# Performance work log

Hardware: AMD Instinct MI355X
Metric: run time of the kernel (lower is better)

Reference implementation:

```python
import jax, jax.numpy as jnp
import numpy as np

N_NODES = 100000
N_EDGES = 1000000
IN_DIM = 64
HID = 64
OUT_DIM = 32
NUM_GRAPHS = 512


def setup_inputs() -> dict:
    key = jax.random.key(0)
    ks = jax.random.split(key, 16)
    x = jax.random.normal(ks[0], (N_NODES, IN_DIM), dtype=jnp.float32)
    edge_index = jax.random.randint(ks[1], (2, N_EDGES), 0, N_NODES, dtype=jnp.int64)
    batch = jnp.sort(jax.random.randint(ks[2], (N_NODES,), 0, NUM_GRAPHS, dtype=jnp.int64))

    def lin(k, i, o):
        s = 1.0 / np.sqrt(i)
        kw, kb = jax.random.split(k)
        return (jax.random.uniform(kw, (i, o), jnp.float32, -s, s),
                jax.random.uniform(kb, (o,), jnp.float32, -s, s))

    W1a, b1a = lin(ks[3], IN_DIM, HID)
    W2a, b2a = lin(ks[4], HID, HID)
    W1b, b1b = lin(ks[5], HID, HID)
    W2b, b2b = lin(ks[6], HID, HID)
    Wp1, bp1 = lin(ks[7], HID, HID)
    Wp2, bp2 = lin(ks[8], HID, OUT_DIM)
    return dict(x=x, edge_index=edge_index, batch=batch,
                W1a=W1a, b1a=b1a, W2a=W2a, b2a=b2a,
                W1b=W1b, b1b=b1b, W2b=W2b, b2b=b2b,
                Wp1=Wp1, bp1=bp1, Wp2=Wp2, bp2=bp2)


def _gin_layer(x, edge_index, W1, b1, W2, b2):
    # GINConv (eps=0): h_i = MLP(x_i + sum_{j->i} x_j)
    src, dst = edge_index[0], edge_index[1]
    agg = jax.ops.segment_sum(x[src], dst, num_segments=N_NODES)  # [N, d]
    h = x + agg
    h = jnp.maximum(h @ W1 + b1, 0.0) @ W2 + b2
    return h


def reference(x, edge_index, batch,
              W1a, b1a, W2a, b2a,
              W1b, b1b, W2b, b2b,
              Wp1, bp1, Wp2, bp2):
    # layer 0 (dropout is identity in eval mode)
    x = _gin_layer(x, edge_index, W1a, b1a, W2a, b2a)
    x = jnp.maximum(x, 0.0)
    # layer 1
    x = _gin_layer(x, edge_index, W1b, b1b, W2b, b2b)
    emb = x  # pre-ReLU embedding of last executed conv
    x = jnp.maximum(x, 0.0)
    # global mean pool over graphs
    sums = jax.ops.segment_sum(x, batch, num_segments=NUM_GRAPHS)  # [G, d]
    cnts = jax.ops.segment_sum(jnp.ones((x.shape[0],), x.dtype), batch, num_segments=NUM_GRAPHS)
    pooled = sums / jnp.maximum(cnts, 1.0)[:, None]
    # post-MLP (dropout identity in eval)
    out = (pooled @ Wp1 + bp1) @ Wp2 + bp2
    return emb, jax.nn.log_softmax(out, axis=1)
```

## Files before the change

kernel.cpp:

```cpp
#include <hip/hip_runtime.h>
#include <math.h>

#define N_NODES 100000
#define N_EDGES 1000000
#define HID 64
#define OUT_DIM 32
#define NUM_GRAPHS 512
#define CAP 48
#define NBUCK 98
#define BCAP 11264
#define ACHUNK 4096

typedef __attribute__((ext_vector_type(4))) float f4v;
typedef __attribute__((ext_vector_type(4))) int i4v;
typedef __attribute__((ext_vector_type(8))) short s8v;
typedef __attribute__((ext_vector_type(4))) short s4vs;

static __device__ inline short f2bf(float f) {
  unsigned u = __float_as_uint(f);
  unsigned r = (u + 0x7fffu + ((u >> 16) & 1u)) >> 16;
  return (short)r;
}
static __device__ inline float bf2f(short s) {
  return __uint_as_float(((unsigned)(unsigned short)s) << 16);
}

__global__ __launch_bounds__(256) void prep_kernel(
    const float* __restrict__ W1a, const float* __restrict__ W2a,
    const float* __restrict__ W1b, const float* __restrict__ W2b,
    short* __restrict__ wtab, const int* __restrict__ batch,
    int* __restrict__ starts, int* __restrict__ bcnt) {
  int t = blockIdx.x * 256 + threadIdx.x;
  if (t < 16384) {
    int which = t >> 12;
    int r = t & 4095;
    const float* W = (which == 0) ? W1a : (which == 1) ? W2a : (which == 2) ? W1b : W2b;
    short* hiT = wtab + which * 8192;
    short* loT = hiT + 4096;
    int n = r & 63, k = r >> 6;
    float w = W[k * HID + n];
    short h = f2bf(w);
    hiT[n * HID + k] = h;
    loT[n * HID + k] = f2bf(w - bf2f(h));
  } else if (t < 16384 + NUM_GRAPHS + 1) {
    int g = t - 16384;
    int lo = 0, hi = N_NODES;
    while (lo < hi) {
      int mid = (lo + hi) >> 1;
      if (batch[mid] < g) lo = mid + 1; else hi = mid;
    }
    starts[g] = lo;
  } else if (t < 16384 + NUM_GRAPHS + 1 + NBUCK) {
    bcnt[t - 16384 - NUM_GRAPHS - 1] = 0;
  }
}

__global__ __launch_bounds__(256) void bucket_kernel(
    const int* __restrict__ ei, int* __restrict__ bedge,
    int* __restrict__ bcnt, int n_edges) {
  __shared__ int s_pack[ACHUNK];
  __shared__ unsigned char s_b[ACHUNK];
  __shared__ int s_sorted[ACHUNK];
  __shared__ int s_hist[NBUCK];
  __shared__ int s_off[NBUCK];
  __shared__ int s_base[NBUCK];

  int e0 = blockIdx.x * ACHUNK;
  int n = n_edges - e0;
  if (n > ACHUNK) n = ACHUNK;
  int tid = threadIdx.x;

  for (int i = tid; i < NBUCK; i += 256) s_hist[i] = 0;
  __syncthreads();

  for (int i = tid; i < n; i += 256) {
    int src = ei[e0 + i];
    int dst = ei[n_edges + e0 + i];
    int b = dst >> 10;
    s_pack[i] = src | ((dst & 1023) << 17);
    s_b[i] = (unsigned char)b;
    atomicAdd(&s_hist[b], 1);
  }
  __syncthreads();

  if (tid < NBUCK) s_off[tid] = s_hist[tid];
  __syncthreads();
  for (int off = 1; off < NBUCK; off <<= 1) {
    int v = 0;
    if (tid < NBUCK && tid >= off) v = s_off[tid - off];
    __syncthreads();
    if (tid < NBUCK && tid >= off) s_off[tid] += v;
    __syncthreads();
  }
  if (tid < NBUCK) {
    int excl = s_off[tid] - s_hist[tid];
    s_off[tid] = excl;
    int c = s_hist[tid];
    s_base[tid] = c > 0 ? atomicAdd(&bcnt[tid], c) : 0;
  }
  __syncthreads();

  for (int i = tid; i < n; i += 256) {
    int p = atomicAdd(&s_off[s_b[i]], 1);
    s_sorted[p] = s_pack[i];
  }
  __syncthreads();

  int wv = tid >> 6;
  int lane = tid & 63;
  for (int b = wv; b < NBUCK; b += 4) {
    int cnt = s_hist[b];
    if (cnt == 0) continue;
    int start = s_off[b] - cnt;
    int gbase = s_base[b];
    for (int i = lane; i < cnt; i += 64) {
      int idx = gbase + i;
      if (idx < BCAP) bedge[b * BCAP + idx] = s_sorted[start + i];
    }
  }
}

__global__ __launch_bounds__(256) void csr_from_buckets_kernel(
    const int* __restrict__ bedge, const int* __restrict__ bcnt,
    int* __restrict__ deg, int* __restrict__ csr) {
  __shared__ int ldeg[1024];
  int b = blockIdx.x;
  int tid = threadIdx.x;
  for (int i = tid; i < 1024; i += 256) ldeg[i] = 0;
  __syncthreads();

  int n = bcnt[b];
  if (n > BCAP) n = BCAP;
  const int* bb = bedge + b * BCAP;
  for (int i0 = tid * 4; i0 < n; i0 += 1024) {
    int e0, e1, e2, e3;
    int rem = n - i0;
    if (rem >= 4) {
      i4v v = *(const i4v*)(bb + i0);
      e0 = v.x; e1 = v.y; e2 = v.z; e3 = v.w;
    } else {
      e0 = bb[i0];
      e1 = (rem > 1) ? bb[i0 + 1] : 0;
      e2 = (rem > 2) ? bb[i0 + 2] : 0;
      e3 = 0;
    }
    {
      int local = e0 >> 17, src = e0 & 0x1FFFF;
      int slot = atomicAdd(&ldeg[local], 1);
      if (slot < CAP) csr[(((size_t)b << 10) | local) * CAP + slot] = src;
    }
    if (n - i0 > 1) {
      int local = e1 >> 17, src = e1 & 0x1FFFF;
      int slot = atomicAdd(&ldeg[local], 1);
      if (slot < CAP) csr[(((size_t)b << 10) | local) * CAP + slot] = src;
    }
    if (n - i0 > 2) {
      int local = e2 >> 17, src = e2 & 0x1FFFF;
      int slot = atomicAdd(&ldeg[local], 1);
      if (slot < CAP) csr[(((size_t)b << 10) | local) * CAP + slot] = src;
    }
    if (n - i0 > 3) {
      int local = e3 >> 17, src = e3 & 0x1FFFF;
      int slot = atomicAdd(&ldeg[local], 1);
      if (slot < CAP) csr[(((size_t)b << 10) | local) * CAP + slot] = src;
    }
  }
  __syncthreads();

  for (int i = tid; i < 1024; i += 256) {
    int node = (b << 10) + i;
    if (node < N_NODES) deg[node] = ldeg[i];
  }
}

__global__ __launch_bounds__(256) void gather_kernel(
    const float* __restrict__ x, const int* __restrict__ deg,
    const int* __restrict__ csr, short* __restrict__ hbufHi,
    short* __restrict__ hbufLo, int n_nodes) {
  int lane = threadIdx.x & 63;
  int node = blockIdx.x * (blockDim.x >> 6) + (threadIdx.x >> 6);
  if (node >= n_nodes) return;
  int g = lane >> 4;
  int sub = lane & 15;

  const f4v* x4 = (const f4v*)x;
  f4v a0 = (g == 0) ? x4[(size_t)node * 16 + sub] : (f4v){0.f, 0.f, 0.f, 0.f};
  int idx = (lane < 16) ? csr[node * CAP + lane] : 0;
  int d = deg[node];
  if (d > CAP) d = CAP;

  f4v a1 = {0.f, 0.f, 0.f, 0.f};
  f4v a2 = {0.f, 0.f, 0.f, 0.f};
  f4v a3 = {0.f, 0.f, 0.f, 0.f};
  if (d > 0) {
    int j1 = g, j2 = 4 + g, j3 = 8 + g, j4 = 12 + g;
    int s1 = __shfl(idx, j1);
    int s2 = __shfl(idx, j2);
    int s3 = __shfl(idx, j3);
    int s4 = __shfl(idx, j4);
    if (j1 < d) a0 += x4[(size_t)s1 * 16 + sub];
    if (j2 < d) a1 += x4[(size_t)s2 * 16 + sub];
    if (j3 < d) a2 += x4[(size_t)s3 * 16 + sub];
    if (j4 < d) a3 += x4[(size_t)s4 * 16 + sub];
  }
  if (d > 16) {
    int idx2 = (lane < 32) ? csr[node * CAP + 16 + lane] : 0;
    for (int j0 = 16; j0 < d; j0 += 16) {
      int j1 = j0 + g, j2 = j0 + 4 + g, j3 = j0 + 8 + g, j4 = j0 + 12 + g;
      int s1 = __shfl(idx2, j1 - 16);
      int s2 = __shfl(idx2, j2 - 16);
      int s3 = __shfl(idx2, j3 - 16);
      int s4 = __shfl(idx2, j4 - 16);
      if (j1 < d) a0 += x4[(size_t)s1 * 16 + sub];
      if (j2 < d) a1 += x4[(size_t)s2 * 16 + sub];
      if (j3 < d) a2 += x4[(size_t)s3 * 16 + sub];
      if (j4 < d) a3 += x4[(size_t)s4 * 16 + sub];
    }
  }
  f4v a = (a0 + a1) + (a2 + a3);
  a.x += __shfl_xor(a.x, 16); a.y += __shfl_xor(a.y, 16);
  a.z += __shfl_xor(a.z, 16); a.w += __shfl_xor(a.w, 16);
  a.x += __shfl_xor(a.x, 32); a.y += __shfl_xor(a.y, 32);
  a.z += __shfl_xor(a.z, 32); a.w += __shfl_xor(a.w, 32);
  if (g == 0) {
    s4vs hi, lo;
#pragma unroll
    for (int c = 0; c < 4; c++) {
      float v = a[c];
      short hb = f2bf(v);
      hi[c] = hb;
      lo[c] = f2bf(v - bf2f(hb));
    }
    ((s4vs*)hbufHi)[(size_t)node * 16 + sub] = hi;
    ((s4vs*)hbufLo)[(size_t)node * 16 + sub] = lo;
  }
}

#define LPAD 72

__global__ __launch_bounds__(256) void gin_mlp_mfma_kernel(
    const short* __restrict__ hbufHi, const short* __restrict__ hbufLo,
    const short* __restrict__ W1hi, const short* __restrict__ W1lo,
    const float* __restrict__ b1,
    const short* __restrict__ W2hi, const short* __restrict__ W2lo,
    const float* __restrict__ b2,
    float* __restrict__ out, int n_nodes, int apply_relu) {
  __shared__ short lds[4][2][16 * LPAD];

  int lane = threadIdx.x & 63;
  int wv = threadIdx.x >> 6;
  int m = lane & 15;
  int quad = lane >> 4;
  int nodeBase = blockIdx.x * 64 + wv * 16;
  int node = nodeBase + m;
  bool valid = node < n_nodes;

  s8v ahi[2], alo[2];
#pragma unroll
  for (int kb = 0; kb < 2; kb++) {
    int off = node * HID + kb * 32 + quad * 8;
    if (valid) {
      ahi[kb] = *(const s8v*)(hbufHi + off);
      alo[kb] = *(const s8v*)(hbufLo + off);
    } else {
      ahi[kb] = (s8v){0, 0, 0, 0, 0, 0, 0, 0};
      alo[kb] = (s8v){0, 0, 0, 0, 0, 0, 0, 0};
    }
  }

  f4v acc[4];
#pragma unroll
  for (int nt = 0; nt < 4; nt++) acc[nt] = (f4v){0.f, 0.f, 0.f, 0.f};
#pragma unroll
  for (int kb = 0; kb < 2; kb++) {
#pragma unroll
    for (int nt = 0; nt < 4; nt++) {
      int n = nt * 16 + m;
      s8v bh = *(const s8v*)(W1hi + n * HID + kb * 32 + quad * 8);
      s8v bl = *(const s8v*)(W1lo + n * HID + kb * 32 + quad * 8);
      acc[nt] = __builtin_amdgcn_mfma_f32_16x16x32_bf16(ahi[kb], bh, acc[nt], 0, 0, 0);
      acc[nt] = __builtin_amdgcn_mfma_f32_16x16x32_bf16(ahi[kb], bl, acc[nt], 0, 0, 0);
      acc[nt] = __builtin_amdgcn_mfma_f32_16x16x32_bf16(alo[kb], bh, acc[nt], 0, 0, 0);
      acc[nt] = __builtin_amdgcn_mfma_f32_16x16x32_bf16(alo[kb], bl, acc[nt], 0, 0, 0);
    }
  }

  short* Lhi = lds[wv][0];
  short* Llo = lds[wv][1];
#pragma unroll
  for (int nt = 0; nt < 4; nt++) {
    int col = nt * 16 + m;
    float bb = b1[col];
#pragma unroll
    for (int r = 0; r < 4; r++) {
      int row = quad * 4 + r;
      float h = fmaxf(acc[nt][r] + bb, 0.f);
      short hb = f2bf(h);
      Lhi[row * LPAD + col] = hb;
      Llo[row * LPAD + col] = f2bf(h - bf2f(hb));
    }
  }
  __syncthreads();

  s8v a2hi[2], a2lo[2];
#pragma unroll
  for (int kb = 0; kb < 2; kb++) {
    int off = m * LPAD + kb * 32 + quad * 8;
    a2hi[kb] = *(const s8v*)(Lhi + off);
    a2lo[kb] = *(const s8v*)(Llo + off);
  }

  f4v acc2[4];
#pragma unroll
  for (int nt = 0; nt < 4; nt++) acc2[nt] = (f4v){0.f, 0.f, 0.f, 0.f};
#pragma unroll
  for (int kb = 0; kb < 2; kb++) {
#pragma unroll
    for (int nt = 0; nt < 4; nt++) {
      int n = nt * 16 + m;
      s8v bh = *(const s8v*)(W2hi + n * HID + kb * 32 + quad * 8);
      s8v bl = *(const s8v*)(W2lo + n * HID + kb * 32 + quad * 8);
      acc2[nt] = __builtin_amdgcn_mfma_f32_16x16x32_bf16(a2hi[kb], bh, acc2[nt], 0, 0, 0);
      acc2[nt] = __builtin_amdgcn_mfma_f32_16x16x32_bf16(a2hi[kb], bl, acc2[nt], 0, 0, 0);
      acc2[nt] = __builtin_amdgcn_mfma_f32_16x16x32_bf16(a2lo[kb], bh, acc2[nt], 0, 0, 0);
      acc2[nt] = __builtin_amdgcn_mfma_f32_16x16x32_bf16(a2lo[kb], bl, acc2[nt], 0, 0, 0);
    }
  }

#pragma unroll
  for (int nt = 0; nt < 4; nt++) {
    int col = nt * 16 + m;
    float bb = b2[col];
#pragma unroll
    for (int r = 0; r < 4; r++) {
      int row = quad * 4 + r;
      int onode = nodeBase + row;
      if (onode < n_nodes) {
        float o = acc2[nt][r] + bb;
        if (apply_relu) o = fmaxf(o, 0.f);
        out[(size_t)onode * HID + col] = o;
      }
    }
  }
}

__global__ __launch_bounds__(256) void poolhead_kernel(
    const float* __restrict__ emb, const int* __restrict__ starts,
    const float* __restrict__ Wp1, const float* __restrict__ bp1,
    const float* __restrict__ Wp2, const float* __restrict__ bp2,
    float* __restrict__ out) {
  int lane = threadIdx.x & 63;
  int g = blockIdx.x * 4 + (threadIdx.x >> 6);
  int group = lane >> 4, sub = lane & 15;
  int s0 = starts[g], s1 = starts[g + 1];

  const f4v* e4 = (const f4v*)emb;
  f4v acc = {0.f, 0.f, 0.f, 0.f};
  for (int n = s0 + group; n < s1; n += 4) {
    f4v v = e4[(size_t)n * 16 + sub];
    v.x = fmaxf(v.x, 0.f); v.y = fmaxf(v.y, 0.f);
    v.z = fmaxf(v.z, 0.f); v.w = fmaxf(v.w, 0.f);
    acc += v;
  }
  acc.x += __shfl_xor(acc.x, 16); acc.y += __shfl_xor(acc.y, 16);
  acc.z += __shfl_xor(acc.z, 16); acc.w += __shfl_xor(acc.w, 16);
  acc.x += __shfl_xor(acc.x, 32); acc.y += __shfl_xor(acc.y, 32);
  acc.z += __shfl_xor(acc.z, 32); acc.w += __shfl_xor(acc.w, 32);
  int srcl = lane >> 2;
  float v0 = __shfl(acc.x, srcl);
  float v1 = __shfl(acc.y, srcl);
  float v2 = __shfl(acc.z, srcl);
  float v3 = __shfl(acc.w, srcl);
  int r = lane & 3;
  float psum = (r == 0) ? v0 : (r == 1) ? v1 : (r == 2) ? v2 : v3;

  float c = fmaxf((float)(s1 - s0), 1.0f);
  float p = psum / c;

  float t = bp1[lane];
#pragma unroll
  for (int k = 0; k < HID; k++) {
    t += __shfl(p, k) * Wp1[k * HID + lane];
  }

  float acc2 = 0.0f;
#pragma unroll
  for (int k = 0; k < HID; k++) {
    float tk = __shfl(t, k);
    if (lane < OUT_DIM) acc2 += tk * Wp2[k * OUT_DIM + lane];
  }
  float o = (lane < OUT_DIM) ? (acc2 + bp2[lane]) : -1e30f;

  float m = o;
#pragma unroll
  for (int off = 32; off >= 1; off >>= 1) m = fmaxf(m, __shfl_xor(m, off));
  float ex = (lane < OUT_DIM) ? expf(o - m) : 0.0f;
  float s = ex;
#pragma unroll
  for (int off = 32; off >= 1; off >>= 1) s += __shfl_xor(s, off);
  float lse = m + logf(s);
  if (lane < OUT_DIM) out[g * OUT_DIM + lane] = o - lse;
}

extern "C" void kernel_launch(void* const* d_in, const int* in_sizes, int n_in,
                              void* d_out, int out_size, void* d_ws, size_t ws_size,
                              hipStream_t stream) {
  const float* x   = (const float*)d_in[0];
  const int* ei    = (const int*)d_in[1];
  const int* batch = (const int*)d_in[2];
  const float* W1a = (const float*)d_in[3];
  const float* b1a = (const float*)d_in[4];
  const float* W2a = (const float*)d_in[5];
  const float* b2a = (const float*)d_in[6];
  const float* W1b = (const float*)d_in[7];
  const float* b1b = (const float*)d_in[8];
  const float* W2b = (const float*)d_in[9];
  const float* b2b = (const float*)d_in[10];
  const float* Wp1 = (const float*)d_in[11];
  const float* bp1 = (const float*)d_in[12];
  const float* Wp2 = (const float*)d_in[13];
  const float* bp2 = (const float*)d_in[14];

  float* emb    = (float*)d_out;
  float* logits = (float*)d_out + (size_t)N_NODES * HID;
  float* x1 = emb;

  short* hbufHi = (short*)d_ws;
  short* hbufLo = hbufHi + (size_t)N_NODES * HID;
  int* bedge   = (int*)d_ws;
  int* bcnt    = bedge + NBUCK * BCAP;
  int* deg     = (int*)((float*)d_ws + (size_t)N_NODES * HID);
  int* csr     = deg + N_NODES;
  int* starts  = csr + (size_t)N_NODES * CAP;
  short* wtab  = (short*)(starts + NUM_GRAPHS + 1);
  short* W1aHi = wtab + 0 * 4096; short* W1aLo = wtab + 1 * 4096;
  short* W2aHi = wtab + 2 * 4096; short* W2aLo = wtab + 3 * 4096;
  short* W1bHi = wtab + 4 * 4096; short* W1bLo = wtab + 5 * 4096;
  short* W2bHi = wtab + 6 * 4096; short* W2bLo = wtab + 7 * 4096;

  int prep_threads = 16384 + (NUM_GRAPHS + 1) + NBUCK;
  prep_kernel<<<(prep_threads + 255) / 256, 256, 0, stream>>>(
      W1a, W2a, W1b, W2b, wtab, batch, starts, bcnt);

  bucket_kernel<<<(N_EDGES + ACHUNK - 1) / ACHUNK, 256, 0, stream>>>(
      ei, bedge, bcnt, N_EDGES);
  csr_from_buckets_kernel<<<NBUCK, 256, 0, stream>>>(bedge, bcnt, deg, csr);

  int gather_blocks = (N_NODES + 3) / 4;
  int mlp_blocks = (N_NODES + 63) / 64;

  gather_kernel<<<gather_blocks, 256, 0, stream>>>(
      x, deg, csr, hbufHi, hbufLo, N_NODES);
  gin_mlp_mfma_kernel<<<mlp_blocks, 256, 0, stream>>>(
      hbufHi, hbufLo, W1aHi, W1aLo, b1a, W2aHi, W2aLo, b2a, x1, N_NODES, 1);

  gather_kernel<<<gather_blocks, 256, 0, stream>>>(
      x1, deg, csr, hbufHi, hbufLo, N_NODES);
  gin_mlp_mfma_kernel<<<mlp_blocks, 256, 0, stream>>>(
      hbufHi, hbufLo, W1bHi, W1bLo, b1b, W2bHi, W2bLo, b2b, emb, N_NODES, 0);

  poolhead_kernel<<<NUM_GRAPHS / 4, 256, 0, stream>>>(
      emb, starts, Wp1, bp1, Wp2, bp2, logits);
}
```

Baseline: 322.7 us.

## Fuse prep into bucket kernel, drop lo*lo MFMA term, one graph per pool block

Merges the weight-split/graph-start prep kernel into the edge bucketing kernel as extra blocks, and replaces the bucket-count zeroing with a memset, saving one launch. Drops the lo×lo cross term from the split-bf16 MFMA products in both MLP layers, cutting a quarter of the matrix instructions at a tiny precision cost. Pool/head kernel now uses one 64-thread block per graph instead of four graphs per 256-thread block.

```diff
diff --git a/kernel.cpp b/kernel.cpp
--- a/kernel.cpp
+++ b/kernel.cpp
@@ -25,39 +25,41 @@
   return __uint_as_float(((unsigned)(unsigned short)s) << 16);
 }
 
-__global__ __launch_bounds__(256) void prep_kernel(
+__global__ __launch_bounds__(256) void bucket_prep_kernel(
+    const int* __restrict__ ei, int* __restrict__ bedge,
+    int* __restrict__ bcnt, int n_edges,
     const float* __restrict__ W1a, const float* __restrict__ W2a,
     const float* __restrict__ W1b, const float* __restrict__ W2b,
     short* __restrict__ wtab, const int* __restrict__ batch,
-    int* __restrict__ starts, int* __restrict__ bcnt) {
-  int t = blockIdx.x * 256 + threadIdx.x;
-  if (t < 16384) {
-    int which = t >> 12;
-    int r = t & 4095;
-    const float* W = (which == 0) ? W1a : (which == 1) ? W2a : (which == 2) ? W1b : W2b;
-    short* hiT = wtab + which * 8192;
-    short* loT = hiT + 4096;
-    int n = r & 63, k = r >> 6;
-    float w = W[k * HID + n];
-    short h = f2bf(w);
-    hiT[n * HID + k] = h;
-    loT[n * HID + k] = f2bf(w - bf2f(h));
-  } else if (t < 16384 + NUM_GRAPHS + 1) {
-    int g = t - 16384;
-    int lo = 0, hi = N_NODES;
-    while (lo < hi) {
-      int mid = (lo + hi) >> 1;
-      if (batch[mid] < g) lo = mid + 1; else hi = mid;
-    }
-    starts[g] = lo;
-  } else if (t < 16384 + NUM_GRAPHS + 1 + NBUCK) {
-    bcnt[t - 16384 - NUM_GRAPHS - 1] = 0;
-  }
-}
-
-__global__ __launch_bounds__(256) void bucket_kernel(
-    const int* __restrict__ ei, int* __restrict__ bedge,
-    int* __restrict__ bcnt, int n_edges) {
+    int* __restrict__ starts) {
+  int nEB = (n_edges + ACHUNK - 1) / ACHUNK;
+  int tid = threadIdx.x;
+
+  if ((int)blockIdx.x >= nEB) {
+    int t = ((int)blockIdx.x - nEB) * 256 + tid;
+    if (t < 16384) {
+      int which = t >> 12;
+      int r = t & 4095;
+      const float* W = (which == 0) ? W1a : (which == 1) ? W2a : (which == 2) ? W1b : W2b;
+      short* hiT = wtab + which * 8192;
+      short* loT = hiT + 4096;
+      int n = r & 63, k = r >> 6;
+      float w = W[k * HID + n];
+      short h = f2bf(w);
+      hiT[n * HID + k] = h;
+      loT[n * HID + k] = f2bf(w - bf2f(h));
+    } else if (t < 16384 + NUM_GRAPHS + 1) {
+      int g = t - 16384;
+      int lo = 0, hi = N_NODES;
+      while (lo < hi) {
+        int mid = (lo + hi) >> 1;
+        if (batch[mid] < g) lo = mid + 1; else hi = mid;
+      }
+      starts[g] = lo;
+    }
+    return;
+  }
+
   __shared__ int s_pack[ACHUNK];
   __shared__ unsigned char s_b[ACHUNK];
   __shared__ int s_sorted[ACHUNK];
@@ -68,7 +70,6 @@
   int e0 = blockIdx.x * ACHUNK;
   int n = n_edges - e0;
   if (n > ACHUNK) n = ACHUNK;
-  int tid = threadIdx.x;
 
   for (int i = tid; i < NBUCK; i += 256) s_hist[i] = 0;
   __syncthreads();
@@ -281,7 +282,6 @@
       acc[nt] = __builtin_amdgcn_mfma_f32_16x16x32_bf16(ahi[kb], bh, acc[nt], 0, 0, 0);
       acc[nt] = __builtin_amdgcn_mfma_f32_16x16x32_bf16(ahi[kb], bl, acc[nt], 0, 0, 0);
       acc[nt] = __builtin_amdgcn_mfma_f32_16x16x32_bf16(alo[kb], bh, acc[nt], 0, 0, 0);
-      acc[nt] = __builtin_amdgcn_mfma_f32_16x16x32_bf16(alo[kb], bl, acc[nt], 0, 0, 0);
     }
   }
 
@@ -323,7 +323,6 @@
       acc2[nt] = __builtin_amdgcn_mfma_f32_16x16x32_bf16(a2hi[kb], bh, acc2[nt], 0, 0, 0);
       acc2[nt] = __builtin_amdgcn_mfma_f32_16x16x32_bf16(a2hi[kb], bl, acc2[nt], 0, 0, 0);
       acc2[nt] = __builtin_amdgcn_mfma_f32_16x16x32_bf16(a2lo[kb], bh, acc2[nt], 0, 0, 0);
-      acc2[nt] = __builtin_amdgcn_mfma_f32_16x16x32_bf16(a2lo[kb], bl, acc2[nt], 0, 0, 0);
     }
   }
 
@@ -344,13 +343,13 @@
   }
 }
 
-__global__ __launch_bounds__(256) void poolhead_kernel(
+__global__ __launch_bounds__(64) void poolhead_kernel(
     const float* __restrict__ emb, const int* __restrict__ starts,
     const float* __restrict__ Wp1, const float* __restrict__ bp1,
     const float* __restrict__ Wp2, const float* __restrict__ bp2,
     float* __restrict__ out) {
   int lane = threadIdx.x & 63;
-  int g = blockIdx.x * 4 + (threadIdx.x >> 6);
+  int g = blockIdx.x;
   int group = lane >> 4, sub = lane & 15;
   int s0 = starts[g], s1 = starts[g + 1];
 
@@ -438,12 +437,12 @@
   short* W1bHi = wtab + 4 * 4096; short* W1bLo = wtab + 5 * 4096;
   short* W2bHi = wtab + 6 * 4096; short* W2bLo = wtab + 7 * 4096;
 
-  int prep_threads = 16384 + (NUM_GRAPHS + 1) + NBUCK;
-  prep_kernel<<<(prep_threads + 255) / 256, 256, 0, stream>>>(
-      W1a, W2a, W1b, W2b, wtab, batch, starts, bcnt);
-
-  bucket_kernel<<<(N_EDGES + ACHUNK - 1) / ACHUNK, 256, 0, stream>>>(
-      ei, bedge, bcnt, N_EDGES);
+  hipMemsetAsync(bcnt, 0, NBUCK * sizeof(int), stream);
+  int nEB = (N_EDGES + ACHUNK - 1) / ACHUNK;
+  int prepB = (16384 + NUM_GRAPHS + 1 + 255) / 256;
+  bucket_prep_kernel<<<nEB + prepB, 256, 0, stream>>>(
+      ei, bedge, bcnt, N_EDGES, W1a, W2a, W1b, W2b, wtab, batch, starts);
+
   csr_from_buckets_kernel<<<NBUCK, 256, 0, stream>>>(bedge, bcnt, deg, csr);
 
   int gather_blocks = (N_NODES + 3) / 4;
@@ -459,6 +458,6 @@
   gin_mlp_mfma_kernel<<<mlp_blocks, 256, 0, stream>>>(
       hbufHi, hbufLo, W1bHi, W1bLo, b1b, W2bHi, W2bLo, b2b, emb, N_NODES, 0);
 
-  poolhead_kernel<<<NUM_GRAPHS / 4, 256, 0, stream>>>(
+  poolhead_kernel<<<NUM_GRAPHS, 64, 0, stream>>>(
       emb, starts, Wp1, bp1, Wp2, bp2, logits);
 }
```

After: 318.2 us. About the same (-1.4%).
